# Optimization experiments

Hardware: AMD Instinct MI355X
Metric: run time of the kernel (lower is better)

Reference implementation:

```python
import jax, jax.numpy as jnp
import numpy as np

STRIDES = (8, 16, 32)
H = W = 640
SCORE_T = 0.5
NMS_T = 0.4


def setup_inputs() -> dict:
    key = jax.random.key(0)
    ks = jax.random.split(key, 9)
    feats = [(H // s) * (W // s) for s in STRIDES]  # 6400, 1600, 400
    d = {}
    for i, n in enumerate(feats):
        d[f"score{i}"] = jax.random.normal(ks[i], (1, n, 1), jnp.float32)
        d[f"bbox{i}"] = jax.random.normal(ks[3 + i], (1, n, 4), jnp.float32)
        d[f"kps{i}"] = jax.random.normal(ks[6 + i], (1, n, 10), jnp.float32)
    return d


def _anchors(stride):
    fh, fw = H // stride, W // stride
    yv, xv = jnp.meshgrid(jnp.arange(fh), jnp.arange(fw), indexing="ij")
    return jnp.stack([xv, yv], -1).reshape(-1, 2).astype(jnp.float32) * stride


def _decode(score, bbox, kps, stride):
    pts = _anchors(stride)                      # [N,2]
    s = jax.nn.sigmoid(score[0]).reshape(-1)    # [N]
    d = bbox[0] * stride                        # [N,4]
    x1 = pts[:, 0] - d[:, 0]
    y1 = pts[:, 1] - d[:, 1]
    x2 = pts[:, 0] + d[:, 2]
    y2 = pts[:, 1] + d[:, 3]
    b = jnp.stack([x1, y1, x2, y2], -1)         # [N,4]
    kd = (kps[0] * stride).reshape(-1, 5, 2)    # [N,5,2] (px,py pairs)
    k = (pts[:, None, :] + kd).reshape(-1, 10)  # [N,10]
    return s, b, k


def _iou(b):
    area = (b[:, 2] - b[:, 0]) * (b[:, 3] - b[:, 1])
    lt = jnp.maximum(b[:, None, :2], b[None, :, :2])
    rb = jnp.minimum(b[:, None, 2:], b[None, :, 2:])
    wh = jnp.clip(rb - lt, 0.0)
    inter = wh[..., 0] * wh[..., 1]
    return inter / (area[:, None] + area[None, :] - inter + 1e-9)


def _nms_keep(iou, valid, thresh):
    # greedy NMS on score-sorted boxes: keep i iff no earlier kept j has IoU>thresh
    n = valid.shape[0]
    def body(keep, xs):
        i, row = xs
        suppressed = jnp.any(keep & (row > thresh))
        keep = keep.at[i].set(valid[i] & ~suppressed)
        return keep, None
    keep, _ = jax.lax.scan(body, jnp.zeros(n, bool), (jnp.arange(n), iou))
    return keep


def reference(score0, score1, score2, bbox0, bbox1, bbox2, kps0, kps1, kps2):
    parts = [
        _decode(s, b, k, st)
        for s, b, k, st in zip(
            (score0, score1, score2), (bbox0, bbox1, bbox2), (kps0, kps1, kps2), STRIDES
        )
    ]
    scores = jnp.concatenate([p[0] for p in parts])  # [8400]
    boxes = jnp.concatenate([p[1] for p in parts])   # [8400,4]
    kpss = jnp.concatenate([p[2] for p in parts])    # [8400,10]
    order = jnp.argsort(-scores)                     # score-descending (NMS order)
    scores = scores[order]
    boxes = boxes[order]
    kpss = kpss[order]
    valid = scores > SCORE_T                         # threshold mask
    iou = _iou(jax.lax.stop_gradient(boxes))         # [8400,8400] ~282MB
    keep = _nms_keep(iou, valid, NMS_T)
    m = keep.astype(boxes.dtype)
    # fixed-shape equivalent of dynamic gather: suppressed rows zeroed, keep mask returned
    return boxes * m[:, None], scores * m, kpss * m[:, None], keep
```

## Files before the change

kernel.cpp:

```cpp
#include <hip/hip_runtime.h>
#include <math.h>

#define N_TOT 8400
#define MASK_WORDS 132
#define CAP 32
#define RT 33

typedef unsigned long long u64;

__device__ __forceinline__ unsigned mono_u32(float f) {
    unsigned u = __float_as_uint(f);
    return (u & 0x80000000u) ? ~u : (u | 0x80000000u);
}

__global__ void decode_kernel(const float* __restrict__ score0, const float* __restrict__ bbox0, const float* __restrict__ kps0,
                              const float* __restrict__ score1, const float* __restrict__ bbox1, const float* __restrict__ kps1,
                              const float* __restrict__ score2, const float* __restrict__ bbox2, const float* __restrict__ kps2,
                              float* __restrict__ logit, float* __restrict__ sig,
                              float* __restrict__ box, float* __restrict__ kps,
                              u64* __restrict__ key, int* __restrict__ rank,
                              unsigned int* __restrict__ cnt,
                              u64* __restrict__ validw, u64* __restrict__ rowflag) {
    int i = blockIdx.x * blockDim.x + threadIdx.x;
    if (i >= N_TOT) return;
    if (i < MASK_WORDS) { validw[i] = 0ull; rowflag[i] = 0ull; }
    rank[i] = 0;
    cnt[i] = 0u;
    const float *sc, *bb, *kp;
    int m, F; float s;
    if (i < 6400)      { sc = score0; bb = bbox0; kp = kps0; m = i;        F = 80; s = 8.f;  }
    else if (i < 8000) { sc = score1; bb = bbox1; kp = kps1; m = i - 6400; F = 40; s = 16.f; }
    else               { sc = score2; bb = bbox2; kp = kps2; m = i - 8000; F = 20; s = 32.f; }
    float px = (float)(m % F) * s;
    float py = (float)(m / F) * s;
    float lg = sc[m];
    logit[i] = lg;
    sig[i] = 1.0f / (1.0f + expf(-lg));
    key[i] = ((u64)(~mono_u32(lg)) << 14) | (u64)i;
    float d0 = bb[m*4+0]*s, d1 = bb[m*4+1]*s, d2 = bb[m*4+2]*s, d3 = bb[m*4+3]*s;
    box[i*4+0] = px - d0;
    box[i*4+1] = py - d1;
    box[i*4+2] = px + d2;
    box[i*4+3] = py + d3;
    #pragma unroll
    for (int c = 0; c < 5; ++c) {
        kps[i*10 + 2*c]   = px + kp[m*10 + 2*c]   * s;
        kps[i*10 + 2*c+1] = py + kp[m*10 + 2*c+1] * s;
    }
}

__global__ __launch_bounds__(256) void rank_kernel(const u64* __restrict__ key, int* __restrict__ rank) {
    __shared__ u64 tile[256];
    int i = blockIdx.x * 256 + threadIdx.x;
    int t0 = blockIdx.y * 256;
    u64 ki = (i < N_TOT) ? key[i] : 0ull;
    int j = t0 + threadIdx.x;
    tile[threadIdx.x] = (j < N_TOT) ? key[j] : ~0ull;
    __syncthreads();
    if (i >= N_TOT) return;
    int rk = 0;
    #pragma unroll 8
    for (int k = 0; k < 256; ++k) {
        rk += (tile[k] < ki) ? 1 : 0;
    }
    if (rk) atomicAdd(&rank[i], rk);
}

__global__ void scatter_kernel(const int* __restrict__ rank,
                               const float* __restrict__ logit, const float* __restrict__ sig,
                               const float* __restrict__ box, const float* __restrict__ kps,
                               float* __restrict__ s_logit, float* __restrict__ s_sig,
                               float* __restrict__ s_box, float* __restrict__ s_kps,
                               u64* __restrict__ validw) {
    int i = blockIdx.x * blockDim.x + threadIdx.x;
    if (i >= N_TOT) return;
    int r = rank[i];
    float lg = logit[i];
    s_logit[r] = lg;
    s_sig[r] = sig[i];
    #pragma unroll
    for (int c = 0; c < 4; ++c)  s_box[r*4+c] = box[i*4+c];
    #pragma unroll
    for (int c = 0; c < 10; ++c) s_kps[r*10+c] = kps[i*10+c];
    if (lg > 0.f) atomicOr(&validw[r >> 6], 1ull << (r & 63));
}

__global__ __launch_bounds__(64) void pairs_kernel(const float* __restrict__ s_logit,
                                                   const float* __restrict__ s_box,
                                                   unsigned int* __restrict__ cnt,
                                                   ulonglong2* __restrict__ ent,
                                                   u64* __restrict__ rowflag) {
    int cw = blockIdx.x;
    int rb = blockIdx.y;
    if (cw < rb) return;
    int tid = threadIdx.x;

    __shared__ float4 cbox[64];
    __shared__ float  carea[64];
    int j0 = cw * 64;
    int j = j0 + tid;
    float4 cb = make_float4(0.f, 0.f, 0.f, 0.f);
    float lgj = -1.f;
    if (j < N_TOT) {
        cb = ((const float4*)s_box)[j];
        lgj = s_logit[j];
    }
    cbox[tid] = cb;
    carea[tid] = (cb.z - cb.x) * (cb.w - cb.y);
    u64 cvalid = __ballot(j < N_TOT && lgj > 0.f);
    __syncthreads();
    if (cvalid == 0ull) return;

    int r = rb * 64 + tid;
    float lgr = (r < N_TOT) ? s_logit[r] : -1.f;
    if (__ballot(lgr > 0.f) == 0ull) return;

    u64 bits = 0ull;
    if (lgr > 0.f) {
        float4 rb4 = ((const float4*)s_box)[r];
        float rarea = (rb4.z - rb4.x) * (rb4.w - rb4.y);
        #pragma unroll 4
        for (int k = 0; k < 64; ++k) {
            float4 c4 = cbox[k];
            float ltx = fmaxf(rb4.x, c4.x);
            float lty = fmaxf(rb4.y, c4.y);
            float rbx = fminf(rb4.z, c4.z);
            float rby = fminf(rb4.w, c4.w);
            float w = fmaxf(rbx - ltx, 0.f);
            float h = fmaxf(rby - lty, 0.f);
            float inter = w * h;
            float iou = inter / (rarea + carea[k] - inter + 1e-9f);
            bits |= (iou > 0.4f) ? (1ull << k) : 0ull;
        }
        u64 m = cvalid;
        if (cw == rb) m &= (tid == 63) ? 0ull : (~0ull << (tid + 1));
        bits &= m;
    }
    if (bits) {
        unsigned idx = atomicAdd(&cnt[r], 1u);
        if (idx < CAP) {
            ulonglong2 e; e.x = bits; e.y = (u64)cw;
            ent[(size_t)r * CAP + idx] = e;
        }
        atomicOr(&rowflag[r >> 6], 1ull << (r & 63));
    }
}

__global__ __launch_bounds__(64) void nms_kernel(const u64* __restrict__ rowflag_g,
                                                 const u64* __restrict__ validw_g,
                                                 const unsigned int* __restrict__ cnt_g,
                                                 const ulonglong2* __restrict__ ent_g,
                                                 u64* __restrict__ keep_words) {
    __shared__ unsigned short list[8448];
    int lane = threadIdx.x;

    u64 rf[3], vw[3];
    #pragma unroll
    for (int s = 0; s < 3; ++s) {
        int w = s * 64 + lane;
        rf[s] = (w < MASK_WORDS) ? rowflag_g[w] : 0ull;
        vw[s] = (w < MASK_WORDS) ? validw_g[w] : 0ull;
    }

    int base = 0;
    #pragma unroll
    for (int s = 0; s < 3; ++s) {
        int c = (int)__popcll(rf[s]);
        int x = c;
        #pragma unroll
        for (int o = 1; o < 64; o <<= 1) { int y = __shfl_up(x, o); if (lane >= o) x += y; }
        int excl = x - c;
        int total = __shfl(x, 63);
        int off = base + excl;
        u64 t = rf[s];
        int wbase = (s * 64 + lane) << 6;
        while (t) {
            int b = __builtin_ctzll(t); t &= t - 1;
            list[off++] = (unsigned short)(wbase | b);
        }
        base += total;
    }
    int n_nz = base;
    __syncthreads();

    u64 rem0 = 0ull, rem1 = 0ull, rem2 = 0ull;

    if (n_nz > 0) {
        int half = lane >> 5;
        int sub  = lane & 31;

        int idx0 = min(sub, n_nz - 1);
        int rowCur = list[idx0];
        unsigned cntCur = cnt_g[rowCur];
        ulonglong2 entCur = ent_g[(size_t)rowCur * CAP + half];

        for (int k0 = 0; k0 < n_nz; k0 += 32) {
            int nb = k0 + 32;
            int rowNxt = 0; unsigned cntNxt = 0u;
            ulonglong2 entNxt; entNxt.x = 0ull; entNxt.y = 0ull;
            if (nb < n_nz) {
                int idx = min(nb + sub, n_nz - 1);
                rowNxt = list[idx];
                cntNxt = cnt_g[rowNxt];
                entNxt = ent_g[(size_t)rowNxt * CAP + half];
            }

            int lim = min(32, n_nz - k0);
            for (int i = 0; i < lim; ++i) {
                int r = __builtin_amdgcn_readlane(rowCur, i);
                int w = r >> 6, slot = w >> 6, owner = w & 63, b = r & 63;
                u64 rw = (slot == 0) ? rem0 : ((slot == 1) ? rem1 : rem2);
                unsigned halfw = (b < 32) ? (unsigned)rw : (unsigned)(rw >> 32);
                unsigned word = (unsigned)__builtin_amdgcn_readlane((int)halfw, owner);
                if (!((word >> (b & 31)) & 1u)) {
                    unsigned c = (unsigned)__builtin_amdgcn_readlane((int)cntCur, i);
                    int ec = (int)min(c, 2u);
                    for (int e = 0; e < ec; ++e) {
                        int src = e * 32 + i;
                        unsigned ey  = (unsigned)__builtin_amdgcn_readlane((int)(unsigned)entCur.y, src);
                        unsigned blo = (unsigned)__builtin_amdgcn_readlane((int)(unsigned)entCur.x, src);
                        unsigned bhi = (unsigned)__builtin_amdgcn_readlane((int)(unsigned)(entCur.x >> 32), src);
                        u64 bits = ((u64)bhi << 32) | (u64)blo;
                        int es = (int)(ey >> 6), eo = (int)(ey & 63u);
                        u64 add = (lane == eo) ? bits : 0ull;
                        if (es == 0) rem0 |= add; else if (es == 1) rem1 |= add; else rem2 |= add;
                    }
                    if (c > 2u) {
                        unsigned cm = min(c, (unsigned)CAP);
                        for (unsigned e = 2; e < cm; ++e) {
                            ulonglong2 g = ent_g[(size_t)r * CAP + e];
                            int es = (int)(g.y >> 6), eo = (int)(g.y & 63u);
                            u64 add = (lane == eo) ? g.x : 0ull;
                            if (es == 0) rem0 |= add; else if (es == 1) rem1 |= add; else rem2 |= add;
                        }
                    }
                }
            }
            rowCur = rowNxt; cntCur = cntNxt; entCur = entNxt;
        }
    }

    u64 rem[3] = {rem0, rem1, rem2};
    #pragma unroll
    for (int s = 0; s < 3; ++s) {
        int w = s * 64 + lane;
        if (w < MASK_WORDS) keep_words[w] = vw[s] & ~rem[s];
    }
}

__global__ void output_kernel(const float* __restrict__ s_sig, const float* __restrict__ s_box,
                              const float* __restrict__ s_kps,
                              const u64* __restrict__ keep_words,
                              float* __restrict__ out) {
    int r = blockIdx.x * blockDim.x + threadIdx.x;
    if (r >= N_TOT) return;
    float m = ((keep_words[r >> 6] >> (r & 63)) & 1ull) ? 1.0f : 0.0f;
    float* ob = out;
    float* os = out + 33600;
    float* okp = out + 42000;
    float* om = out + 126000;
    #pragma unroll
    for (int c = 0; c < 4; ++c)  ob[r*4+c] = s_box[r*4+c] * m;
    os[r] = s_sig[r] * m;
    #pragma unroll
    for (int c = 0; c < 10; ++c) okp[r*10+c] = s_kps[r*10+c] * m;
    om[r] = m;
}

extern "C" void kernel_launch(void* const* d_in, const int* in_sizes, int n_in,
                              void* d_out, int out_size, void* d_ws, size_t ws_size,
                              hipStream_t stream) {
    const float *score0, *bbox0, *kps0, *score1, *bbox1, *kps1, *score2, *bbox2, *kps2;
    if (in_sizes[1] == 25600) {
        score0 = (const float*)d_in[0]; bbox0 = (const float*)d_in[1]; kps0 = (const float*)d_in[2];
        score1 = (const float*)d_in[3]; bbox1 = (const float*)d_in[4]; kps1 = (const float*)d_in[5];
        score2 = (const float*)d_in[6]; bbox2 = (const float*)d_in[7]; kps2 = (const float*)d_in[8];
    } else {
        score0 = (const float*)d_in[0]; score1 = (const float*)d_in[1]; score2 = (const float*)d_in[2];
        bbox0  = (const float*)d_in[3]; bbox1  = (const float*)d_in[4]; bbox2  = (const float*)d_in[5];
        kps0   = (const float*)d_in[6]; kps1   = (const float*)d_in[7]; kps2   = (const float*)d_in[8];
    }

    char* ws = (char*)d_ws;
    float* logit   = (float*)(ws + 0);
    float* sig     = (float*)(ws + 33600);
    float* box     = (float*)(ws + 67200);
    float* kps     = (float*)(ws + 201600);
    int*   rank    = (int*)  (ws + 537600);
    float* s_logit = (float*)(ws + 571200);
    float* s_sig   = (float*)(ws + 604800);
    float* s_box   = (float*)(ws + 638400);
    float* s_kps   = (float*)(ws + 772800);
    u64*   keep_words = (u64*)(ws + 1108800);
    u64*   validw     = (u64*)(ws + 1110144);
    u64*   rowflag    = (u64*)(ws + 1111296);
    unsigned int* cnt = (unsigned int*)(ws + 1112448);
    u64*   key        = (u64*)(ws + 1146368);
    ulonglong2*   ent = (ulonglong2*)(ws + 1213568);

    float* out = (float*)d_out;

    decode_kernel<<<(N_TOT + 255) / 256, 256, 0, stream>>>(
        score0, bbox0, kps0, score1, bbox1, kps1, score2, bbox2, kps2,
        logit, sig, box, kps, key, rank, cnt, validw, rowflag);
    rank_kernel<<<dim3(RT, RT), 256, 0, stream>>>(key, rank);
    scatter_kernel<<<33, 256, 0, stream>>>(rank, logit, sig, box, kps,
                                           s_logit, s_sig, s_box, s_kps, validw);
    pairs_kernel<<<dim3(MASK_WORDS, MASK_WORDS), 64, 0, stream>>>(s_logit, s_box, cnt, ent, rowflag);
    nms_kernel<<<1, 64, 0, stream>>>(rowflag, validw, cnt, ent, keep_words);
    output_kernel<<<33, 256, 0, stream>>>(s_sig, s_box, s_kps, keep_words, out);
}
```

Measured before the change: 107.9 us.

## Restrict pair IoU grid to valid prefix and fuse NMS with output

Scatter counts the valid (score above threshold) boxes, and since they form a sorted prefix, the pairs kernel launches a fixed persistent grid. That grid walks only the upper-triangular tiles covering the valid prefix, instead of a 132x132 grid that mostly exits early. Column boxes are broadcast with wave shuffles rather than shared memory. The NMS kernel is fused with output writing in one 256-thread block, which removes a launch but makes the output pass run in a single workgroup.

```diff
diff --git a/kernel.cpp b/kernel.cpp
--- a/kernel.cpp
+++ b/kernel.cpp
@@ -5,6 +5,7 @@
 #define MASK_WORDS 132
 #define CAP 32
 #define RT 33
+#define PBLK 256
 
 typedef unsigned long long u64;
 
@@ -20,9 +21,11 @@
                               float* __restrict__ box, float* __restrict__ kps,
                               u64* __restrict__ key, int* __restrict__ rank,
                               unsigned int* __restrict__ cnt,
-                              u64* __restrict__ validw, u64* __restrict__ rowflag) {
+                              u64* __restrict__ validw, u64* __restrict__ rowflag,
+                              int* __restrict__ nvalid) {
     int i = blockIdx.x * blockDim.x + threadIdx.x;
     if (i >= N_TOT) return;
+    if (i == 0) *nvalid = 0;
     if (i < MASK_WORDS) { validw[i] = 0ull; rowflag[i] = 0ull; }
     rank[i] = 0;
     cnt[i] = 0u;
@@ -66,205 +69,213 @@
     if (rk) atomicAdd(&rank[i], rk);
 }
 
-__global__ void scatter_kernel(const int* __restrict__ rank,
+__global__ __launch_bounds__(256) void scatter_kernel(const int* __restrict__ rank,
                                const float* __restrict__ logit, const float* __restrict__ sig,
                                const float* __restrict__ box, const float* __restrict__ kps,
                                float* __restrict__ s_logit, float* __restrict__ s_sig,
                                float* __restrict__ s_box, float* __restrict__ s_kps,
-                               u64* __restrict__ validw) {
+                               u64* __restrict__ validw, int* __restrict__ nvalid) {
     int i = blockIdx.x * blockDim.x + threadIdx.x;
-    if (i >= N_TOT) return;
-    int r = rank[i];
-    float lg = logit[i];
-    s_logit[r] = lg;
-    s_sig[r] = sig[i];
-    #pragma unroll
-    for (int c = 0; c < 4; ++c)  s_box[r*4+c] = box[i*4+c];
-    #pragma unroll
-    for (int c = 0; c < 10; ++c) s_kps[r*10+c] = kps[i*10+c];
-    if (lg > 0.f) atomicOr(&validw[r >> 6], 1ull << (r & 63));
-}
-
-__global__ __launch_bounds__(64) void pairs_kernel(const float* __restrict__ s_logit,
-                                                   const float* __restrict__ s_box,
-                                                   unsigned int* __restrict__ cnt,
-                                                   ulonglong2* __restrict__ ent,
-                                                   u64* __restrict__ rowflag) {
-    int cw = blockIdx.x;
-    int rb = blockIdx.y;
-    if (cw < rb) return;
-    int tid = threadIdx.x;
-
-    __shared__ float4 cbox[64];
-    __shared__ float  carea[64];
-    int j0 = cw * 64;
-    int j = j0 + tid;
-    float4 cb = make_float4(0.f, 0.f, 0.f, 0.f);
-    float lgj = -1.f;
-    if (j < N_TOT) {
-        cb = ((const float4*)s_box)[j];
-        lgj = s_logit[j];
-    }
-    cbox[tid] = cb;
-    carea[tid] = (cb.z - cb.x) * (cb.w - cb.y);
-    u64 cvalid = __ballot(j < N_TOT && lgj > 0.f);
-    __syncthreads();
-    if (cvalid == 0ull) return;
-
-    int r = rb * 64 + tid;
-    float lgr = (r < N_TOT) ? s_logit[r] : -1.f;
-    if (__ballot(lgr > 0.f) == 0ull) return;
-
-    u64 bits = 0ull;
-    if (lgr > 0.f) {
-        float4 rb4 = ((const float4*)s_box)[r];
+    float lg = -1.f;
+    if (i < N_TOT) {
+        int r = rank[i];
+        lg = logit[i];
+        s_logit[r] = lg;
+        s_sig[r] = sig[i];
+        #pragma unroll
+        for (int c = 0; c < 4; ++c)  s_box[r*4+c] = box[i*4+c];
+        #pragma unroll
+        for (int c = 0; c < 10; ++c) s_kps[r*10+c] = kps[i*10+c];
+        if (lg > 0.f) atomicOr(&validw[r >> 6], 1ull << (r & 63));
+    }
+    u64 vb = __ballot(lg > 0.f);
+    if ((threadIdx.x & 63) == 0 && vb) atomicAdd(nvalid, (int)__popcll(vb));
+}
+
+__global__ __launch_bounds__(256) void pairs_kernel(const float* __restrict__ s_logit,
+                                                    const float* __restrict__ s_box,
+                                                    const int* __restrict__ nvalid,
+                                                    unsigned int* __restrict__ cnt,
+                                                    ulonglong2* __restrict__ ent,
+                                                    u64* __restrict__ rowflag) {
+    int wv = threadIdx.x >> 6;
+    int lane = threadIdx.x & 63;
+    int wgid = blockIdx.x * 4 + wv;
+    const int V = *nvalid;
+    const int nw = (V + 63) >> 6;
+    const int T = nw * (nw + 1) / 2;
+    const float4* sbox4 = (const float4*)s_box;
+
+    for (int t = wgid; t < T; t += PBLK * 4) {
+        float fn = (float)nw + 0.5f;
+        int rb = (int)(fn - sqrtf(fn * fn - 2.0f * (float)t));
+        if (rb < 0) rb = 0;
+        while (rb > 0 && (rb * nw - (rb * (rb - 1)) / 2) > t) --rb;
+        while (((rb + 1) * nw - ((rb + 1) * rb) / 2) <= t) ++rb;
+        int cw = rb + (t - (rb * nw - (rb * (rb - 1)) / 2));
+
+        int j = cw * 64 + lane;
+        float4 cb = make_float4(0.f, 0.f, 0.f, 0.f);
+        bool cval = (j < V);
+        if (j < N_TOT) cb = sbox4[j];
+        u64 cvalid = __ballot(cval);
+
+        int r = rb * 64 + lane;
+        bool rval = (r < V);
+
+        float4 rb4 = (r < N_TOT) ? sbox4[r] : make_float4(0.f, 0.f, 0.f, 0.f);
         float rarea = (rb4.z - rb4.x) * (rb4.w - rb4.y);
+        float ca = (cb.z - cb.x) * (cb.w - cb.y);
+        u64 bits = 0ull;
         #pragma unroll 4
         for (int k = 0; k < 64; ++k) {
-            float4 c4 = cbox[k];
-            float ltx = fmaxf(rb4.x, c4.x);
-            float lty = fmaxf(rb4.y, c4.y);
-            float rbx = fminf(rb4.z, c4.z);
-            float rby = fminf(rb4.w, c4.w);
+            float cx1 = __shfl(cb.x, k);
+            float cy1 = __shfl(cb.y, k);
+            float cx2 = __shfl(cb.z, k);
+            float cy2 = __shfl(cb.w, k);
+            float cak = __shfl(ca, k);
+            float ltx = fmaxf(rb4.x, cx1);
+            float lty = fmaxf(rb4.y, cy1);
+            float rbx = fminf(rb4.z, cx2);
+            float rby = fminf(rb4.w, cy2);
             float w = fmaxf(rbx - ltx, 0.f);
             float h = fmaxf(rby - lty, 0.f);
             float inter = w * h;
-            float iou = inter / (rarea + carea[k] - inter + 1e-9f);
+            float iou = inter / (rarea + cak - inter + 1e-9f);
             bits |= (iou > 0.4f) ? (1ull << k) : 0ull;
         }
         u64 m = cvalid;
-        if (cw == rb) m &= (tid == 63) ? 0ull : (~0ull << (tid + 1));
-        bits &= m;
-    }
-    if (bits) {
-        unsigned idx = atomicAdd(&cnt[r], 1u);
-        if (idx < CAP) {
-            ulonglong2 e; e.x = bits; e.y = (u64)cw;
-            ent[(size_t)r * CAP + idx] = e;
-        }
-        atomicOr(&rowflag[r >> 6], 1ull << (r & 63));
-    }
-}
-
-__global__ __launch_bounds__(64) void nms_kernel(const u64* __restrict__ rowflag_g,
-                                                 const u64* __restrict__ validw_g,
-                                                 const unsigned int* __restrict__ cnt_g,
-                                                 const ulonglong2* __restrict__ ent_g,
-                                                 u64* __restrict__ keep_words) {
-    __shared__ unsigned short list[8448];
-    int lane = threadIdx.x;
-
-    u64 rf[3], vw[3];
-    #pragma unroll
-    for (int s = 0; s < 3; ++s) {
-        int w = s * 64 + lane;
-        rf[s] = (w < MASK_WORDS) ? rowflag_g[w] : 0ull;
-        vw[s] = (w < MASK_WORDS) ? validw_g[w] : 0ull;
-    }
-
-    int base = 0;
-    #pragma unroll
-    for (int s = 0; s < 3; ++s) {
-        int c = (int)__popcll(rf[s]);
-        int x = c;
-        #pragma unroll
-        for (int o = 1; o < 64; o <<= 1) { int y = __shfl_up(x, o); if (lane >= o) x += y; }
-        int excl = x - c;
-        int total = __shfl(x, 63);
-        int off = base + excl;
-        u64 t = rf[s];
-        int wbase = (s * 64 + lane) << 6;
-        while (t) {
-            int b = __builtin_ctzll(t); t &= t - 1;
-            list[off++] = (unsigned short)(wbase | b);
-        }
-        base += total;
-    }
-    int n_nz = base;
-    __syncthreads();
-
-    u64 rem0 = 0ull, rem1 = 0ull, rem2 = 0ull;
-
-    if (n_nz > 0) {
-        int half = lane >> 5;
-        int sub  = lane & 31;
-
-        int idx0 = min(sub, n_nz - 1);
-        int rowCur = list[idx0];
-        unsigned cntCur = cnt_g[rowCur];
-        ulonglong2 entCur = ent_g[(size_t)rowCur * CAP + half];
-
-        for (int k0 = 0; k0 < n_nz; k0 += 32) {
-            int nb = k0 + 32;
-            int rowNxt = 0; unsigned cntNxt = 0u;
-            ulonglong2 entNxt; entNxt.x = 0ull; entNxt.y = 0ull;
-            if (nb < n_nz) {
-                int idx = min(nb + sub, n_nz - 1);
-                rowNxt = list[idx];
-                cntNxt = cnt_g[rowNxt];
-                entNxt = ent_g[(size_t)rowNxt * CAP + half];
+        if (cw == rb) m &= (lane == 63) ? 0ull : (~0ull << (lane + 1));
+        bits &= rval ? m : 0ull;
+
+        if (bits) {
+            unsigned idx = atomicAdd(&cnt[r], 1u);
+            if (idx < CAP) {
+                ulonglong2 e; e.x = bits; e.y = (u64)cw;
+                ent[(size_t)r * CAP + idx] = e;
             }
-
-            int lim = min(32, n_nz - k0);
-            for (int i = 0; i < lim; ++i) {
-                int r = __builtin_amdgcn_readlane(rowCur, i);
-                int w = r >> 6, slot = w >> 6, owner = w & 63, b = r & 63;
-                u64 rw = (slot == 0) ? rem0 : ((slot == 1) ? rem1 : rem2);
-                unsigned halfw = (b < 32) ? (unsigned)rw : (unsigned)(rw >> 32);
-                unsigned word = (unsigned)__builtin_amdgcn_readlane((int)halfw, owner);
-                if (!((word >> (b & 31)) & 1u)) {
-                    unsigned c = (unsigned)__builtin_amdgcn_readlane((int)cntCur, i);
-                    int ec = (int)min(c, 2u);
-                    for (int e = 0; e < ec; ++e) {
-                        int src = e * 32 + i;
-                        unsigned ey  = (unsigned)__builtin_amdgcn_readlane((int)(unsigned)entCur.y, src);
-                        unsigned blo = (unsigned)__builtin_amdgcn_readlane((int)(unsigned)entCur.x, src);
-                        unsigned bhi = (unsigned)__builtin_amdgcn_readlane((int)(unsigned)(entCur.x >> 32), src);
-                        u64 bits = ((u64)bhi << 32) | (u64)blo;
-                        int es = (int)(ey >> 6), eo = (int)(ey & 63u);
-                        u64 add = (lane == eo) ? bits : 0ull;
-                        if (es == 0) rem0 |= add; else if (es == 1) rem1 |= add; else rem2 |= add;
-                    }
-                    if (c > 2u) {
-                        unsigned cm = min(c, (unsigned)CAP);
-                        for (unsigned e = 2; e < cm; ++e) {
-                            ulonglong2 g = ent_g[(size_t)r * CAP + e];
-                            int es = (int)(g.y >> 6), eo = (int)(g.y & 63u);
-                            u64 add = (lane == eo) ? g.x : 0ull;
+            atomicOr(&rowflag[r >> 6], 1ull << (r & 63));
+        }
+    }
+}
+
+__global__ __launch_bounds__(256) void nms_output_kernel(const u64* __restrict__ rowflag_g,
+                                                         const u64* __restrict__ validw_g,
+                                                         const unsigned int* __restrict__ cnt_g,
+                                                         const ulonglong2* __restrict__ ent_g,
+                                                         const float* __restrict__ s_sig,
+                                                         const float* __restrict__ s_box,
+                                                         const float* __restrict__ s_kps,
+                                                         float* __restrict__ out) {
+    __shared__ unsigned short nlist[8448];
+    __shared__ u64 keepw[MASK_WORDS];
+    int tid = threadIdx.x;
+
+    if (tid < 64) {
+        int lane = tid;
+        u64 rf[3], vw[3];
+        #pragma unroll
+        for (int s = 0; s < 3; ++s) {
+            int w = s * 64 + lane;
+            rf[s] = (w < MASK_WORDS) ? rowflag_g[w] : 0ull;
+            vw[s] = (w < MASK_WORDS) ? validw_g[w] : 0ull;
+        }
+        int base = 0;
+        #pragma unroll
+        for (int s = 0; s < 3; ++s) {
+            int c = (int)__popcll(rf[s]);
+            int x = c;
+            #pragma unroll
+            for (int o = 1; o < 64; o <<= 1) { int y = __shfl_up(x, o); if (lane >= o) x += y; }
+            int excl = x - c;
+            int total = __shfl(x, 63);
+            int off = base + excl;
+            u64 t = rf[s];
+            int wbase = (s * 64 + lane) << 6;
+            while (t) {
+                int b = __builtin_ctzll(t); t &= t - 1;
+                nlist[off++] = (unsigned short)(wbase | b);
+            }
+            base += total;
+        }
+        int n_nz = base;
+
+        u64 rem0 = 0ull, rem1 = 0ull, rem2 = 0ull;
+        if (n_nz > 0) {
+            int half = lane >> 5;
+            int sub  = lane & 31;
+            int idx0 = min(sub, n_nz - 1);
+            int rowCur = nlist[idx0];
+            unsigned cntCur = cnt_g[rowCur];
+            ulonglong2 entCur = ent_g[(size_t)rowCur * CAP + half];
+
+            for (int k0 = 0; k0 < n_nz; k0 += 32) {
+                int nb = k0 + 32;
+                int rowNxt = 0; unsigned cntNxt = 0u;
+                ulonglong2 entNxt; entNxt.x = 0ull; entNxt.y = 0ull;
+                if (nb < n_nz) {
+                    int idx = min(nb + sub, n_nz - 1);
+                    rowNxt = nlist[idx];
+                    cntNxt = cnt_g[rowNxt];
+                    entNxt = ent_g[(size_t)rowNxt * CAP + half];
+                }
+                int lim = min(32, n_nz - k0);
+                for (int i = 0; i < lim; ++i) {
+                    int r = __builtin_amdgcn_readlane(rowCur, i);
+                    int w = r >> 6, slot = w >> 6, owner = w & 63, b = r & 63;
+                    u64 rw = (slot == 0) ? rem0 : ((slot == 1) ? rem1 : rem2);
+                    unsigned halfw = (b < 32) ? (unsigned)rw : (unsigned)(rw >> 32);
+                    unsigned word = (unsigned)__builtin_amdgcn_readlane((int)halfw, owner);
+                    if (!((word >> (b & 31)) & 1u)) {
+                        unsigned c = (unsigned)__builtin_amdgcn_readlane((int)cntCur, i);
+                        int ec = (int)min(c, 2u);
+                        for (int e = 0; e < ec; ++e) {
+                            int src = e * 32 + i;
+                            unsigned ey  = (unsigned)__builtin_amdgcn_readlane((int)(unsigned)entCur.y, src);
+                            unsigned blo = (unsigned)__builtin_amdgcn_readlane((int)(unsigned)entCur.x, src);
+                            unsigned bhi = (unsigned)__builtin_amdgcn_readlane((int)(unsigned)(entCur.x >> 32), src);
+                            u64 bits = ((u64)bhi << 32) | (u64)blo;
+                            int es = (int)(ey >> 6), eo = (int)(ey & 63u);
+                            u64 add = (lane == eo) ? bits : 0ull;
                             if (es == 0) rem0 |= add; else if (es == 1) rem1 |= add; else rem2 |= add;
+                        }
+                        if (c > 2u) {
+                            unsigned cm = min(c, (unsigned)CAP);
+                            for (unsigned e = 2; e < cm; ++e) {
+                                ulonglong2 g = ent_g[(size_t)r * CAP + e];
+                                int es = (int)(g.y >> 6), eo = (int)(g.y & 63u);
+                                u64 add = (lane == eo) ? g.x : 0ull;
+                                if (es == 0) rem0 |= add; else if (es == 1) rem1 |= add; else rem2 |= add;
+                            }
                         }
                     }
                 }
+                rowCur = rowNxt; cntCur = cntNxt; entCur = entNxt;
             }
-            rowCur = rowNxt; cntCur = cntNxt; entCur = entNxt;
-        }
-    }
-
-    u64 rem[3] = {rem0, rem1, rem2};
-    #pragma unroll
-    for (int s = 0; s < 3; ++s) {
-        int w = s * 64 + lane;
-        if (w < MASK_WORDS) keep_words[w] = vw[s] & ~rem[s];
-    }
-}
-
-__global__ void output_kernel(const float* __restrict__ s_sig, const float* __restrict__ s_box,
-                              const float* __restrict__ s_kps,
-                              const u64* __restrict__ keep_words,
-                              float* __restrict__ out) {
-    int r = blockIdx.x * blockDim.x + threadIdx.x;
-    if (r >= N_TOT) return;
-    float m = ((keep_words[r >> 6] >> (r & 63)) & 1ull) ? 1.0f : 0.0f;
+        }
+        u64 rem[3] = {rem0, rem1, rem2};
+        #pragma unroll
+        for (int s = 0; s < 3; ++s) {
+            int w = s * 64 + lane;
+            if (w < MASK_WORDS) keepw[w] = vw[s] & ~rem[s];
+        }
+    }
+    __syncthreads();
+
     float* ob = out;
     float* os = out + 33600;
     float* okp = out + 42000;
     float* om = out + 126000;
-    #pragma unroll
-    for (int c = 0; c < 4; ++c)  ob[r*4+c] = s_box[r*4+c] * m;
-    os[r] = s_sig[r] * m;
-    #pragma unroll
-    for (int c = 0; c < 10; ++c) okp[r*10+c] = s_kps[r*10+c] * m;
-    om[r] = m;
+    for (int r = tid; r < N_TOT; r += 256) {
+        float m = ((keepw[r >> 6] >> (r & 63)) & 1ull) ? 1.0f : 0.0f;
+        float4 b4 = ((const float4*)s_box)[r];
+        b4.x *= m; b4.y *= m; b4.z *= m; b4.w *= m;
+        ((float4*)ob)[r] = b4;
+        os[r] = s_sig[r] * m;
+        #pragma unroll
+        for (int c = 0; c < 10; ++c) okp[r*10+c] = s_kps[r*10+c] * m;
+        om[r] = m;
+    }
 }
 
 extern "C" void kernel_launch(void* const* d_in, const int* in_sizes, int n_in,
@@ -294,19 +305,21 @@
     u64*   keep_words = (u64*)(ws + 1108800);
     u64*   validw     = (u64*)(ws + 1110144);
     u64*   rowflag    = (u64*)(ws + 1111296);
+    int*   nvalid     = (int*)(ws + 1112384);
     unsigned int* cnt = (unsigned int*)(ws + 1112448);
     u64*   key        = (u64*)(ws + 1146368);
     ulonglong2*   ent = (ulonglong2*)(ws + 1213568);
+    (void)keep_words;
 
     float* out = (float*)d_out;
 
     decode_kernel<<<(N_TOT + 255) / 256, 256, 0, stream>>>(
         score0, bbox0, kps0, score1, bbox1, kps1, score2, bbox2, kps2,
-        logit, sig, box, kps, key, rank, cnt, validw, rowflag);
+        logit, sig, box, kps, key, rank, cnt, validw, rowflag, nvalid);
     rank_kernel<<<dim3(RT, RT), 256, 0, stream>>>(key, rank);
     scatter_kernel<<<33, 256, 0, stream>>>(rank, logit, sig, box, kps,
-                                           s_logit, s_sig, s_box, s_kps, validw);
-    pairs_kernel<<<dim3(MASK_WORDS, MASK_WORDS), 64, 0, stream>>>(s_logit, s_box, cnt, ent, rowflag);
-    nms_kernel<<<1, 64, 0, stream>>>(rowflag, validw, cnt, ent, keep_words);
-    output_kernel<<<33, 256, 0, stream>>>(s_sig, s_box, s_kps, keep_words, out);
-}
+                                           s_logit, s_sig, s_box, s_kps, validw, nvalid);
+    pairs_kernel<<<PBLK, 256, 0, stream>>>(s_logit, s_box, nvalid, cnt, ent, rowflag);
+    nms_output_kernel<<<1, 256, 0, stream>>>(rowflag, validw, cnt, ent,
+                                             s_sig, s_box, s_kps, out);
+}
```

Measured after the change: 135.5 us. +25.6%, slower.
